# Optimization experiments

Hardware: AMD Instinct MI355X
Metric: run time of the kernel (lower is better)

Reference implementation:

```python
import jax, jax.numpy as jnp
import numpy as np
from jax import lax

TAU = 10.0
THR = 1.0
ALPHA = float(np.exp(-1.0 / TAU))  # leak factor exp(-dt/tau), dt=1


def conv2d(x, w, pad):
    # x: [N,C,H,W], w: [O,I,kh,kw]
    return lax.conv_general_dilated(
        x, w, window_strides=(1, 1), padding=[(pad, pad), (pad, pad)],
        dimension_numbers=('NCHW', 'OIHW', 'NCHW'))


def avgpool(x, k):
    n, c, h, w = x.shape
    return x.reshape(n, c, h // k, k, w // k, k).mean(axis=(3, 5))


def exp_leak(x):
    # x: [T, ...]; v[t] = alpha*v[t-1] + x[t]; outputs membrane each step
    def step(v, xt):
        v = ALPHA * v + xt
        return v, v
    _, y = lax.scan(step, jnp.zeros_like(x[0]), x)
    return y


def lif(x):
    # LIF with SingleSpike + MembraneSubtract reset (norm_input=False)
    def step(v, xt):
        v = ALPHA * v + xt
        s = (v >= THR).astype(v.dtype)
        return v - s * THR, s
    _, s = lax.scan(step, jnp.zeros_like(x[0]), x)
    return s


def forward(x, conv1_w, conv2_w, lin_w):
    B, T = x.shape[:2]
    h = avgpool(conv2d(x.reshape(B * T, 2, 32, 32), conv1_w, 2), 4)  # [BT,4,8,8]
    h = h.reshape(B, T, 4, 8, 8).swapaxes(0, 1)                       # [T,B,4,8,8]
    h = lif(exp_leak(h)).swapaxes(0, 1).reshape(B * T, 4, 8, 8)
    h = avgpool(conv2d(h, conv2_w, 1), 2)                             # [BT,8,4,4]
    h = h.reshape(B, T, 8, 4, 4).swapaxes(0, 1)                       # [T,B,8,4,4]
    h = lif(exp_leak(h)).swapaxes(0, 1).reshape(B, T, 8 * 4 * 4)      # [B,T,128]
    return jnp.einsum('btf,of->bto', h, lin_w)                        # [B,T,2]


def setup_inputs() -> dict:
    key = jax.random.key(0)
    k1, k2, k3, k4 = jax.random.split(key, 4)
    B, T = 128, 100
    x = jax.random.uniform(k1, (B, T, 2, 32, 32), dtype=jnp.float32)
    conv1_w = jax.random.normal(k2, (4, 2, 5, 5), dtype=jnp.float32) / np.sqrt(2 * 5 * 5)
    conv2_w = jax.random.normal(k3, (8, 4, 3, 3), dtype=jnp.float32) / np.sqrt(4 * 3 * 3)
    lin_w = jax.random.normal(k4, (2, 128), dtype=jnp.float32) / np.sqrt(128)
    return {'x': x, 'conv1_w': conv1_w, 'conv2_w': conv2_w, 'lin_w': lin_w}


def reference(x, conv1_w, conv2_w, lin_w):
    return forward(x, conv1_w, conv2_w, lin_w)
```

## Files before the change

kernel.cpp:

```cpp
#include <hip/hip_runtime.h>

#define ALPHA 0.90483741803595957f

__global__ void prep_weights(const float* __restrict__ w1, const float* __restrict__ w2,
                             float* __restrict__ w1e, float* __restrict__ w2e) {
    int idx = blockIdx.x * 256 + threadIdx.x;
    if (idx < 512) {
        int v = idx & 7, u = (idx >> 3) & 7, ch = (idx >> 6) & 1, oc = idx >> 7;
        float s = 0.f;
        for (int a = 0; a < 5; ++a) {
            int i = u - a; if (i < 0 || i > 3) continue;
            for (int b = 0; b < 5; ++b) {
                int j = v - b; if (j < 0 || j > 3) continue;
                s += w1[((oc * 2 + ch) * 5 + a) * 5 + b];
            }
        }
        w1e[idx] = s * (1.f / 16.f);
    } else if (idx < 1024) {
        int k = idx - 512;
        int v = k & 3, u = (k >> 2) & 3, ch = (k >> 4) & 3, oc = k >> 6;
        float s = 0.f;
        for (int a = 0; a < 3; ++a) {
            int i = u - a; if (i < 0 || i > 1) continue;
            for (int b = 0; b < 3; ++b) {
                int j = v - b; if (j < 0 || j > 1) continue;
                s += w2[((oc * 4 + ch) * 3 + a) * 3 + b];
            }
        }
        w2e[k] = s * 0.25f;
    }
}

__global__ __launch_bounds__(256) void conv1_pool(const float* __restrict__ x,
                                                  const float* __restrict__ w1e,
                                                  float* __restrict__ y1) {
    __shared__ __align__(16) float tile[4][2][36][36];
    int tid = threadIdx.x;

    float4* t4 = (float4*)&tile[0][0][0][0];
    #pragma unroll
    for (int k = 0; k < 11; ++k) {
        int i = tid + k * 256;
        if (i < 2592) t4[i] = make_float4(0.f, 0.f, 0.f, 0.f);
    }
    __syncthreads();

    int li = tid >> 6, pos = tid & 63;
    long gi = (long)blockIdx.x * 4 + li;
    const float* src = x + gi * 2048;
    #pragma unroll
    for (int k = 0; k < 8; ++k) {
        int e = k * 256 + pos * 4;
        float4 d = *(const float4*)(src + e);
        int ch = e >> 10, rem = e & 1023, r = rem >> 5, c = rem & 31;
        float* dst = &tile[li][ch][r + 2][c + 2];
        dst[0] = d.x; dst[1] = d.y; dst[2] = d.z; dst[3] = d.w;
    }
    __syncthreads();

    int p = pos >> 3, q = pos & 7;
    float acc0 = 0.f, acc1 = 0.f, acc2 = 0.f, acc3 = 0.f;
    #pragma unroll
    for (int ch = 0; ch < 2; ++ch) {
        #pragma unroll
        for (int r = 0; r < 8; ++r) {
            const float* row = &tile[li][ch][4 * p + r][4 * q];
            float4 a = *(const float4*)row;
            float4 b = *(const float4*)(row + 4);
            float in[8] = {a.x, a.y, a.z, a.w, b.x, b.y, b.z, b.w};
            #pragma unroll
            for (int c = 0; c < 8; ++c) {
                float xi = in[c];
                acc0 += w1e[((0 * 2 + ch) * 8 + r) * 8 + c] * xi;
                acc1 += w1e[((1 * 2 + ch) * 8 + r) * 8 + c] * xi;
                acc2 += w1e[((2 * 2 + ch) * 8 + r) * 8 + c] * xi;
                acc3 += w1e[((3 * 2 + ch) * 8 + r) * 8 + c] * xi;
            }
        }
    }
    float* dst = y1 + gi * 256 + pos;
    dst[0] = acc0; dst[64] = acc1; dst[128] = acc2; dst[192] = acc3;
}

__global__ void scan1(const float* __restrict__ y1, float* __restrict__ spk) {
    int idx = blockIdx.x * 256 + threadIdx.x;
    int b = idx >> 8, f = idx & 255;
    const float* p = y1 + (long)b * 100 * 256 + f;
    float* o = spk + (long)b * 100 * 256 + f;
    float v1 = 0.f, v2 = 0.f;
    float xt = p[0];
    #pragma unroll 5
    for (int t = 0; t < 100; ++t) {
        float xn = (t < 99) ? p[(t + 1) * 256] : 0.f;
        v1 = ALPHA * v1 + xt;
        v2 = ALPHA * v2 + v1;
        float s = (v2 >= 1.f) ? 1.f : 0.f;
        o[t * 256] = s;
        v2 -= s;
        xt = xn;
    }
}

__global__ __launch_bounds__(256) void conv2_pool(const float* __restrict__ spk,
                                                  const float* __restrict__ w2e,
                                                  float* __restrict__ y2) {
    __shared__ __align__(16) float tile[2][4][10][10];
    int tid = threadIdx.x;
    float4* t4 = (float4*)&tile[0][0][0][0];
    if (tid < 200) t4[tid] = make_float4(0.f, 0.f, 0.f, 0.f);
    __syncthreads();

    const float* src = spk + (long)blockIdx.x * 512;
    #pragma unroll
    for (int k = 0; k < 2; ++k) {
        int e = k * 256 + tid;
        float d = src[e];
        int li = e >> 8, f = e & 255, ch = f >> 6, rem = f & 63, r = rem >> 3, c = rem & 7;
        tile[li][ch][r + 1][c + 1] = d;
    }
    __syncthreads();

    int li = tid >> 7, tpos = tid & 127;
    int oc = tpos >> 4, p = (tpos >> 2) & 3, q = tpos & 3;
    float acc = 0.f;
    #pragma unroll
    for (int ch = 0; ch < 4; ++ch) {
        #pragma unroll
        for (int r = 0; r < 4; ++r) {
            const float* row = &tile[li][ch][2 * p + r][2 * q];
            #pragma unroll
            for (int c = 0; c < 4; ++c)
                acc += w2e[((oc * 4 + ch) * 4 + r) * 4 + c] * row[c];
        }
    }
    long gi = (long)blockIdx.x * 2 + li;
    y2[gi * 128 + tpos] = acc;
}

__global__ void scan2(const float* __restrict__ y2, float* __restrict__ s2) {
    int idx = blockIdx.x * 256 + threadIdx.x;
    int b = idx >> 7, f = idx & 127;
    const float* p = y2 + (long)b * 100 * 128 + f;
    float* o = s2 + (long)b * 100 * 128 + f;
    float v1 = 0.f, v2 = 0.f;
    float xt = p[0];
    #pragma unroll 5
    for (int t = 0; t < 100; ++t) {
        float xn = (t < 99) ? p[(t + 1) * 128] : 0.f;
        v1 = ALPHA * v1 + xt;
        v2 = ALPHA * v2 + v1;
        float s = (v2 >= 1.f) ? 1.f : 0.f;
        o[t * 128] = s;
        v2 -= s;
        xt = xn;
    }
}

__global__ __launch_bounds__(256) void linear_out(const float* __restrict__ s2,
                                                  const float* __restrict__ lw,
                                                  float* __restrict__ out) {
    int tid = threadIdx.x;
    long bt = (long)blockIdx.x * 4 + (tid >> 6);
    int lane = tid & 63;
    float2 v = *(const float2*)(s2 + bt * 128 + lane * 2);
    float w00 = lw[lane * 2], w01 = lw[lane * 2 + 1];
    float w10 = lw[128 + lane * 2], w11 = lw[128 + lane * 2 + 1];
    float a0 = v.x * w00 + v.y * w01;
    float a1 = v.x * w10 + v.y * w11;
    #pragma unroll
    for (int off = 32; off; off >>= 1) {
        a0 += __shfl_down(a0, off);
        a1 += __shfl_down(a1, off);
    }
    if (lane == 0) { out[bt * 2] = a0; out[bt * 2 + 1] = a1; }
}

extern "C" void kernel_launch(void* const* d_in, const int* in_sizes, int n_in,
                              void* d_out, int out_size, void* d_ws, size_t ws_size,
                              hipStream_t stream) {
    const float* x  = (const float*)d_in[0];
    const float* w1 = (const float*)d_in[1];
    const float* w2 = (const float*)d_in[2];
    const float* lw = (const float*)d_in[3];
    float* out = (float*)d_out;

    float* ws   = (float*)d_ws;
    float* w1e  = ws;
    float* w2e  = ws + 512;
    float* bufA = ws + 1024;
    float* bufB = bufA + 3276800;

    prep_weights<<<4, 256, 0, stream>>>(w1, w2, w1e, w2e);
    conv1_pool<<<3200, 256, 0, stream>>>(x, w1e, bufA);
    scan1<<<128, 256, 0, stream>>>(bufA, bufB);
    conv2_pool<<<6400, 256, 0, stream>>>(bufB, w2e, bufA);
    scan2<<<64, 256, 0, stream>>>(bufA, bufB);
    linear_out<<<3200, 256, 0, stream>>>(bufB, lw, out);
}
```

Baseline: 211.3 us.

## Fuse scan1, conv2+pool, scan2 and linear into one per-batch kernel

Replaces four kernels (scan1, conv2_pool, scan2, linear_out) with one kernel that runs one block per batch element and steps through time. Each step computes the layer-1 LIF spike into shared memory, then the pooled conv2, the second LIF and the linear reduction. This removes the intermediate spike and activation buffers and three launches. In exchange it runs only 128 blocks with two barriers per timestep, a serial critical path with low occupancy.

```diff
diff --git a/kernel.cpp b/kernel.cpp
--- a/kernel.cpp
+++ b/kernel.cpp
@@ -82,97 +82,88 @@
     dst[0] = acc0; dst[64] = acc1; dst[128] = acc2; dst[192] = acc3;
 }
 
-__global__ void scan1(const float* __restrict__ y1, float* __restrict__ spk) {
-    int idx = blockIdx.x * 256 + threadIdx.x;
-    int b = idx >> 8, f = idx & 255;
-    const float* p = y1 + (long)b * 100 * 256 + f;
-    float* o = spk + (long)b * 100 * 256 + f;
-    float v1 = 0.f, v2 = 0.f;
-    float xt = p[0];
-    #pragma unroll 5
+__global__ __launch_bounds__(256) void fused_tail(const float* __restrict__ y1,
+                                                  const float* __restrict__ w2e,
+                                                  const float* __restrict__ lw,
+                                                  float* __restrict__ out) {
+    __shared__ float tile[4][10][10];
+    __shared__ float red[2][2];
+    int tid = threadIdx.x;
+    int b = blockIdx.x;
+
+    for (int i = tid; i < 400; i += 256) ((float*)tile)[i] = 0.f;
+
+    int ch1 = tid >> 6, r1 = (tid >> 3) & 7, c1 = tid & 7;
+    float* tslot = &tile[ch1][r1 + 1][c1 + 1];
+
+    int oc = tid >> 4, p = (tid >> 2) & 3, q = tid & 3;
+    float wts[64];
+    float lw0 = 0.f, lw1 = 0.f;
+    if (tid < 128) {
+        #pragma unroll
+        for (int k = 0; k < 64; ++k) wts[k] = w2e[oc * 64 + k];
+        lw0 = lw[tid];
+        lw1 = lw[128 + tid];
+    }
+    const float* base = &tile[0][2 * p][2 * q];
+
+    const float* src = y1 + (long)b * 100 * 256 + tid;
+    float* outp = out + (long)b * 200;
+
+    float cur = src[0];
+    float nxt = src[256];
+    float v1 = 0.f, v2 = 0.f, v1b = 0.f, v2b = 0.f;
+
+    __syncthreads();
+
     for (int t = 0; t < 100; ++t) {
-        float xn = (t < 99) ? p[(t + 1) * 256] : 0.f;
-        v1 = ALPHA * v1 + xt;
+        float nn = (t + 2 < 100) ? src[(t + 2) * 256] : 0.f;
+
+        v1 = ALPHA * v1 + cur;
         v2 = ALPHA * v2 + v1;
         float s = (v2 >= 1.f) ? 1.f : 0.f;
-        o[t * 256] = s;
         v2 -= s;
-        xt = xn;
+        *tslot = s;
+        __syncthreads();
+
+        if (tid < 128) {
+            float acc = 0.f;
+            #pragma unroll
+            for (int ch = 0; ch < 4; ++ch) {
+                #pragma unroll
+                for (int r = 0; r < 4; ++r) {
+                    const float* row = base + ch * 100 + r * 10;
+                    float2 u = *(const float2*)row;
+                    float2 w = *(const float2*)(row + 2);
+                    acc += wts[ch * 16 + r * 4 + 0] * u.x;
+                    acc += wts[ch * 16 + r * 4 + 1] * u.y;
+                    acc += wts[ch * 16 + r * 4 + 2] * w.x;
+                    acc += wts[ch * 16 + r * 4 + 3] * w.y;
+                }
+            }
+            v1b = ALPHA * v1b + acc;
+            v2b = ALPHA * v2b + v1b;
+            float s2 = (v2b >= 1.f) ? 1.f : 0.f;
+            v2b -= s2;
+
+            float a0 = s2 * lw0;
+            float a1 = s2 * lw1;
+            #pragma unroll
+            for (int off = 32; off; off >>= 1) {
+                a0 += __shfl_xor(a0, off);
+                a1 += __shfl_xor(a1, off);
+            }
+            if ((tid & 63) == 0) { red[tid >> 6][0] = a0; red[tid >> 6][1] = a1; }
+        }
+        __syncthreads();
+        if (tid == 0) {
+            float2 o2;
+            o2.x = red[0][0] + red[1][0];
+            o2.y = red[0][1] + red[1][1];
+            *(float2*)(outp + t * 2) = o2;
+        }
+        cur = nxt; nxt = nn;
     }
-}
-
-__global__ __launch_bounds__(256) void conv2_pool(const float* __restrict__ spk,
-                                                  const float* __restrict__ w2e,
-                                                  float* __restrict__ y2) {
-    __shared__ __align__(16) float tile[2][4][10][10];
-    int tid = threadIdx.x;
-    float4* t4 = (float4*)&tile[0][0][0][0];
-    if (tid < 200) t4[tid] = make_float4(0.f, 0.f, 0.f, 0.f);
-    __syncthreads();
-
-    const float* src = spk + (long)blockIdx.x * 512;
-    #pragma unroll
-    for (int k = 0; k < 2; ++k) {
-        int e = k * 256 + tid;
-        float d = src[e];
-        int li = e >> 8, f = e & 255, ch = f >> 6, rem = f & 63, r = rem >> 3, c = rem & 7;
-        tile[li][ch][r + 1][c + 1] = d;
-    }
-    __syncthreads();
-
-    int li = tid >> 7, tpos = tid & 127;
-    int oc = tpos >> 4, p = (tpos >> 2) & 3, q = tpos & 3;
-    float acc = 0.f;
-    #pragma unroll
-    for (int ch = 0; ch < 4; ++ch) {
-        #pragma unroll
-        for (int r = 0; r < 4; ++r) {
-            const float* row = &tile[li][ch][2 * p + r][2 * q];
-            #pragma unroll
-            for (int c = 0; c < 4; ++c)
-                acc += w2e[((oc * 4 + ch) * 4 + r) * 4 + c] * row[c];
-        }
-    }
-    long gi = (long)blockIdx.x * 2 + li;
-    y2[gi * 128 + tpos] = acc;
-}
-
-__global__ void scan2(const float* __restrict__ y2, float* __restrict__ s2) {
-    int idx = blockIdx.x * 256 + threadIdx.x;
-    int b = idx >> 7, f = idx & 127;
-    const float* p = y2 + (long)b * 100 * 128 + f;
-    float* o = s2 + (long)b * 100 * 128 + f;
-    float v1 = 0.f, v2 = 0.f;
-    float xt = p[0];
-    #pragma unroll 5
-    for (int t = 0; t < 100; ++t) {
-        float xn = (t < 99) ? p[(t + 1) * 128] : 0.f;
-        v1 = ALPHA * v1 + xt;
-        v2 = ALPHA * v2 + v1;
-        float s = (v2 >= 1.f) ? 1.f : 0.f;
-        o[t * 128] = s;
-        v2 -= s;
-        xt = xn;
-    }
-}
-
-__global__ __launch_bounds__(256) void linear_out(const float* __restrict__ s2,
-                                                  const float* __restrict__ lw,
-                                                  float* __restrict__ out) {
-    int tid = threadIdx.x;
-    long bt = (long)blockIdx.x * 4 + (tid >> 6);
-    int lane = tid & 63;
-    float2 v = *(const float2*)(s2 + bt * 128 + lane * 2);
-    float w00 = lw[lane * 2], w01 = lw[lane * 2 + 1];
-    float w10 = lw[128 + lane * 2], w11 = lw[128 + lane * 2 + 1];
-    float a0 = v.x * w00 + v.y * w01;
-    float a1 = v.x * w10 + v.y * w11;
-    #pragma unroll
-    for (int off = 32; off; off >>= 1) {
-        a0 += __shfl_down(a0, off);
-        a1 += __shfl_down(a1, off);
-    }
-    if (lane == 0) { out[bt * 2] = a0; out[bt * 2 + 1] = a1; }
 }
 
 extern "C" void kernel_launch(void* const* d_in, const int* in_sizes, int n_in,
@@ -187,13 +178,9 @@
     float* ws   = (float*)d_ws;
     float* w1e  = ws;
     float* w2e  = ws + 512;
-    float* bufA = ws + 1024;
-    float* bufB = bufA + 3276800;
+    float* y1   = ws + 1024;
 
     prep_weights<<<4, 256, 0, stream>>>(w1, w2, w1e, w2e);
-    conv1_pool<<<3200, 256, 0, stream>>>(x, w1e, bufA);
-    scan1<<<128, 256, 0, stream>>>(bufA, bufB);
-    conv2_pool<<<6400, 256, 0, stream>>>(bufB, w2e, bufA);
-    scan2<<<64, 256, 0, stream>>>(bufA, bufB);
-    linear_out<<<3200, 256, 0, stream>>>(bufB, lw, out);
+    conv1_pool<<<3200, 256, 0, stream>>>(x, w1e, y1);
+    fused_tail<<<128, 256, 0, stream>>>(y1, w2e, lw, out);
 }
```

Result: slower. 250.0 us (+18.3%).
